# Performance work log

Measured on AMD Instinct MI355X. Metric: run time of the kernel, lower is better.

Reference implementation:

```python
import jax, jax.numpy as jnp
import numpy as np

LN_EPS = 1e-5

def _layernorm(x, g, b):
    mu = jnp.mean(x, axis=-1, keepdims=True)
    var = jnp.var(x, axis=-1, keepdims=True)
    return (x - mu) * jax.lax.rsqrt(var + LN_EPS) * g + b

def _attention(q_in, ctx, wq, wk, wv, wo, bo, n_heads):
    b, n, _ = q_in.shape
    m = ctx.shape[1]
    d_attn = wq.shape[1]
    d_head = d_attn // n_heads
    Q = (q_in @ wq).reshape(b, n, n_heads, d_head)
    K = (ctx @ wk).reshape(b, m, n_heads, d_head)
    V = (ctx @ wv).reshape(b, m, n_heads, d_head)
    scale = 1.0 / np.sqrt(d_head).astype(np.float32)
    sim = jnp.einsum('bnhd,bmhd->bhnm', Q, K) * scale
    attn = jax.nn.softmax(sim, axis=-1)
    out = jnp.einsum('bhnm,bmhd->bnhd', attn, V).reshape(b, n, d_attn)
    return out @ wo + bo

def setup_inputs() -> dict:
    key = jax.random.key(0)
    ks = jax.random.split(key, 16)
    B, N, D = 8, 1024, 640
    M, CD = 77, 768
    H = 4 * D  # GEGLU hidden = 2560
    s = lambda d: 1.0 / np.sqrt(d)
    return {
        'x': jax.random.normal(ks[0], (B, N, D), jnp.float32),
        'context': jax.random.normal(ks[1], (B, M, CD), jnp.float32),
        'sa_wq': jax.random.normal(ks[2], (D, D), jnp.float32) * s(D),
        'sa_wk': jax.random.normal(ks[3], (D, D), jnp.float32) * s(D),
        'sa_wv': jax.random.normal(ks[4], (D, D), jnp.float32) * s(D),
        'sa_wo': jax.random.normal(ks[5], (D, D), jnp.float32) * s(D),
        'sa_bo': jnp.zeros((D,), jnp.float32),
        'ca_wq': jax.random.normal(ks[6], (D, D), jnp.float32) * s(D),
        'ca_wk': jax.random.normal(ks[7], (CD, D), jnp.float32) * s(CD),
        'ca_wv': jax.random.normal(ks[8], (CD, D), jnp.float32) * s(CD),
        'ca_wo': jax.random.normal(ks[9], (D, D), jnp.float32) * s(D),
        'ca_bo': jnp.zeros((D,), jnp.float32),
        'ff_w1': jax.random.normal(ks[10], (D, 2 * H), jnp.float32) * s(D),
        'ff_b1': jnp.zeros((2 * H,), jnp.float32),
        'ff_w2': jax.random.normal(ks[11], (H, D), jnp.float32) * s(H),
        'ff_b2': jnp.zeros((D,), jnp.float32),
        'ln1_g': jnp.ones((D,), jnp.float32), 'ln1_b': jnp.zeros((D,), jnp.float32),
        'ln2_g': jnp.ones((D,), jnp.float32), 'ln2_b': jnp.zeros((D,), jnp.float32),
        'ln3_g': jnp.ones((D,), jnp.float32), 'ln3_b': jnp.zeros((D,), jnp.float32),
    }

def reference(x, context, sa_wq, sa_wk, sa_wv, sa_wo, sa_bo,
              ca_wq, ca_wk, ca_wv, ca_wo, ca_bo,
              ff_w1, ff_b1, ff_w2, ff_b2,
              ln1_g, ln1_b, ln2_g, ln2_b, ln3_g, ln3_b):
    n_heads = 8
    # post-norm residual block, matching norm_i(x + sublayer(x))
    x = _layernorm(x + _attention(x, x, sa_wq, sa_wk, sa_wv, sa_wo, sa_bo, n_heads), ln1_g, ln1_b)
    x = _layernorm(x + _attention(x, context, ca_wq, ca_wk, ca_wv, ca_wo, ca_bo, n_heads), ln2_g, ln2_b)
    h = x @ ff_w1 + ff_b1
    a, gate = jnp.split(h, 2, axis=-1)
    ff = (a * jax.nn.gelu(gate, approximate=False)) @ ff_w2 + ff_b2
    x = _layernorm(x + ff, ln3_g, ln3_b)
    return x
```

## Files before the change

kernel.cpp:

```cpp
#include <hip/hip_runtime.h>


using u16 = unsigned short;
typedef __attribute__((ext_vector_type(8))) short bfrag;
typedef __attribute__((ext_vector_type(4))) float f4;
typedef __attribute__((ext_vector_type(4))) unsigned short us4;

#define MFMA(a, b, c) __builtin_amdgcn_mfma_f32_16x16x32_bf16((a), (b), (c), 0, 0, 0)

__device__ __forceinline__ void gload16(const void* g, void* l) {
    __builtin_amdgcn_global_load_lds(
        (const __attribute__((address_space(1))) void*)g,
        (__attribute__((address_space(3))) void*)l, 16, 0, 0);
}

__device__ __forceinline__ u16 f2b(float f) {
    unsigned u = __float_as_uint(f);
    unsigned r = u + 0x7FFFu + ((u >> 16) & 1u);
    return (u16)(r >> 16);
}
__device__ __forceinline__ float b2f(u16 u) {
    return __uint_as_float(((unsigned)u) << 16);
}
__device__ __forceinline__ unsigned pack2(float a, float b) {
    return (unsigned)f2b(a) | ((unsigned)f2b(b) << 16);
}
__device__ __forceinline__ bfrag bzero() {
    bfrag z = {0,0,0,0,0,0,0,0};
    return z;
}
__device__ __forceinline__ float gelu_f(float x) {
    float y = 0.7978845608028654f * (x + 0.044715f * x * x * x);
    float e = exp2f(y * 2.8853900817779268f);
    float t = 1.0f - 2.0f * __builtin_amdgcn_rcpf(e + 1.0f);
    return 0.5f * x * (1.0f + t);
}

__device__ __forceinline__ void transp_tile(const float* __restrict__ in,
                                            u16* __restrict__ out,
                                            int K, int N, int ldo,
                                            int tile, bool perm,
                                            float (*t)[33])
{
    int nw = N >> 5;
    int n0 = (tile % nw) * 32, k0 = (tile / nw) * 32;
    int tx = threadIdx.x & 31, ty = threadIdx.x >> 5;
    #pragma unroll
    for (int i = 0; i < 32; i += 8)
        t[ty + i][tx] = in[(size_t)(k0 + ty + i) * N + n0 + tx];
    __syncthreads();
    #pragma unroll
    for (int i = 0; i < 32; i += 8) {
        int n = n0 + ty + i;
        int dst;
        if (perm) {
            dst = (n < 2560) ? ((n >> 5) * 64 + (n & 31))
                             : (((n - 2560) >> 5) * 64 + 32 + ((n - 2560) & 31));
        } else {
            dst = n;
        }
        out[(size_t)dst * ldo + k0 + tx] = f2b(t[tx][ty + i]);
    }
}

__global__ __launch_bounds__(256) void prep_k(
    const float* __restrict__ x, const float* __restrict__ ctx,
    const float* __restrict__ sa_wq, const float* __restrict__ sa_wk,
    const float* __restrict__ sa_wv, const float* __restrict__ sa_wo,
    const float* __restrict__ ca_wq, const float* __restrict__ ca_wk,
    const float* __restrict__ ca_wv, const float* __restrict__ ca_wo,
    const float* __restrict__ ff_w1, const float* __restrict__ ff_w2,
    u16* saqkvt, u16* sawot, u16* cawqt, u16* cawot, u16* cakvt,
    u16* ffw1t, u16* ffw2t, u16* xb, u16* ctxb)
{
    __shared__ float t[32][33];
    int b = blockIdx.x;
    if (b < 2400) {
        int task = b / 400, tile = b - task * 400;
        const float* src;
        u16* dst;
        if      (task == 0) { src = sa_wq; dst = saqkvt; }
        else if (task == 1) { src = sa_wk; dst = saqkvt + 409600; }
        else if (task == 2) { src = sa_wv; dst = saqkvt + 819200; }
        else if (task == 3) { src = sa_wo; dst = sawot; }
        else if (task == 4) { src = ca_wq; dst = cawqt; }
        else                { src = ca_wo; dst = cawot; }
        transp_tile(src, dst, 640, 640, 640, tile, false, t);
    } else if (b < 3360) {
        int tt = b - 2400;
        int task = tt / 480, tile = tt - task * 480;
        transp_tile(task ? ca_wv : ca_wk, cakvt + task * 491520, 768, 640, 768,
                    tile, false, t);
    } else if (b < 6560) {
        transp_tile(ff_w1, ffw1t, 640, 5120, 640, b - 3360, true, t);
    } else if (b < 8160) {
        transp_tile(ff_w2, ffw2t, 2560, 640, 2560, b - 6560, false, t);
    } else if (b < 10720) {
        int i = (b - 8160) * 256 + threadIdx.x;
        const float4* p = (const float4*)x + (size_t)i * 2;
        float4 a = p[0], bb = p[1];
        uint4 w = { pack2(a.x, a.y), pack2(a.z, a.w),
                    pack2(bb.x, bb.y), pack2(bb.z, bb.w) };
        ((uint4*)xb)[i] = w;
    } else {
        int i = (b - 10720) * 256 + threadIdx.x;
        int rowOut = i / 96, c8 = (i - rowOut * 96) * 8;
        int bb = rowOut / 80, r = rowOut - bb * 80;
        uint4 w = {0, 0, 0, 0};
        if (r < 77) {
            const float4* p = (const float4*)(ctx + ((size_t)(bb * 77 + r)) * 768 + c8);
            float4 a = p[0], b2 = p[1];
            w = (uint4){ pack2(a.x, a.y), pack2(a.z, a.w),
                         pack2(b2.x, b2.y), pack2(b2.z, b2.w) };
        }
        ((uint4*)ctxb)[i] = w;
    }
}

template<int MODE>
__device__ __forceinline__ void gemm_core(const u16* __restrict__ A,
                                          const u16* __restrict__ Bt,
                                          int N, int K, int ld,
                                          const float* __restrict__ bias,
                                          const u16* __restrict__ resb,
                                          float* __restrict__ outf,
                                          u16* __restrict__ outb,
                                          u16* __restrict__ out2,
                                          int bx, int by,
                                          u16* As, u16* Bs)
{
    const int lane = threadIdx.x & 63;
    const int wid  = threadIdx.x >> 6;
    const int q    = lane >> 4;
    const int lc   = lane & 15;
    const int wm = wid >> 1, wn = wid & 1;
    const int m0 = by * 128;
    const int n0 = bx * 128;
    const int ldb = ld * 2;

    f4 acc[4][4];
    #pragma unroll
    for (int i = 0; i < 4; ++i)
        #pragma unroll
        for (int j = 0; j < 4; ++j) acc[i][j] = (f4){0.f, 0.f, 0.f, 0.f};

    const char* Abase = (const char*)A + (size_t)m0 * ldb;
    const char* Bbase = (const char*)Bt + (size_t)n0 * ldb;

    for (int kt = 0; kt < K; kt += 64) {
        #pragma unroll
        for (int c = 0; c < 4; ++c) {
            int cid = wid * 4 + c;
            int o = cid * 1024 + lane * 16;
            int row = o >> 7;
            int pc  = o & 127;
            int src = pc ^ ((row & 7) << 4);
            gload16(Abase + (size_t)row * ldb + kt * 2 + src, (char*)As + cid * 1024);
            gload16(Bbase + (size_t)row * ldb + kt * 2 + src, (char*)Bs + cid * 1024);
        }
        __syncthreads();
        #pragma unroll
        for (int ks = 0; ks < 2; ++ks) {
            bfrag a[4], b[4];
            #pragma unroll
            for (int mi = 0; mi < 4; ++mi) {
                int row = wm * 64 + mi * 16 + lc;
                int off = row * 128 + ((ks * 64 + q * 16) ^ ((row & 7) << 4));
                a[mi] = *(const bfrag*)((const char*)As + off);
            }
            #pragma unroll
            for (int ni = 0; ni < 4; ++ni) {
                int row = wn * 64 + ni * 16 + lc;
                int off = row * 128 + ((ks * 64 + q * 16) ^ ((row & 7) << 4));
                b[ni] = *(const bfrag*)((const char*)Bs + off);
            }
            #pragma unroll
            for (int mi = 0; mi < 4; ++mi)
                #pragma unroll
                for (int ni = 0; ni < 4; ++ni)
                    acc[mi][ni] = MFMA(a[mi], b[ni], acc[mi][ni]);
        }
        __syncthreads();
    }

    const int baseRow = m0 + wm * 64;
    const int baseCol = n0 + wn * 64;

    if (MODE == 4) {
        const int blk = baseCol >> 6;
        #pragma unroll
        for (int mi = 0; mi < 4; ++mi)
            #pragma unroll
            for (int ni = 0; ni < 2; ++ni) {
                int j = blk * 32 + ni * 16 + lc;
                float ba = bias[j];
                float bg = bias[2560 + j];
                #pragma unroll
                for (int r = 0; r < 4; ++r) {
                    int row = baseRow + mi * 16 + q * 4 + r;
                    float aa = acc[mi][ni][r] + ba;
                    float gg = acc[mi][ni + 2][r] + bg;
                    outb[(size_t)row * 2560 + j] = f2b(aa * gelu_f(gg));
                }
            }
        return;
    }

    #pragma unroll
    for (int mi = 0; mi < 4; ++mi)
        #pragma unroll
        for (int ni = 0; ni < 4; ++ni) {
            int col = baseCol + ni * 16 + lc;
            if (MODE == 2) {
                const float qs = (col < 640) ? 0.11180339887498949f : 1.0f;
                us4 vv = {0, 0, 0, 0};
                #pragma unroll
                for (int r = 0; r < 4; ++r) {
                    int row = baseRow + mi * 16 + q * 4 + r;
                    u16 u = f2b(acc[mi][ni][r] * qs);
                    outb[(size_t)row * 1920 + col] = u;
                    vv[r] = u;
                }
                if (col >= 1280) {
                    int cd = col - 1280;
                    int hh = cd / 80, dd = cd - hh * 80;
                    int row0 = baseRow + mi * 16 + q * 4;
                    int bb = row0 >> 10, tok = row0 & 1023;
                    *(us4*)&out2[(size_t)((bb * 8 + hh) * 80 + dd) * 1024 + tok] = vv;
                }
            } else {
                #pragma unroll
                for (int r = 0; r < 4; ++r) {
                    int row = baseRow + mi * 16 + q * 4 + r;
                    float v = acc[mi][ni][r];
                    if (MODE == 1) {
                        outb[(size_t)row * N + col] = f2b(v);
                    } else if (MODE == 3) {
                        int bb = row / 80, rr = row - bb * 80;
                        if (rr < 77) {
                            u16 u = f2b(v);
                            if (col < 640) {
                                outb[(size_t)row * 640 + col] = u;
                            } else {
                                int cd = col - 640;
                                int hh = cd / 80, dd = cd - hh * 80;
                                out2[((bb * 8 + hh) * 80 + dd) * 80 + rr] = u;
                            }
                        }
                    }
                }
            }
        }
}

template<int MODE>
__global__ __launch_bounds__(256) void gemm_bt(const u16* __restrict__ A,
                                               const u16* __restrict__ Bt,
                                               int N, int K,
                                               const float* __restrict__ bias,
                                               const u16* __restrict__ resb,
                                               float* __restrict__ outf,
                                               u16* __restrict__ outb,
                                               u16* __restrict__ out2)
{
    __shared__ u16 As[128 * 64];
    __shared__ u16 Bs[128 * 64];
    gemm_core<MODE>(A, Bt, N, K, K, bias, resb, outf, outb, out2,
                    blockIdx.x, blockIdx.y, As, Bs);
}

__global__ __launch_bounds__(256) void gemm_qkv_cakv(
    const u16* __restrict__ xb, const u16* __restrict__ saqkvt,
    const u16* __restrict__ ctxb, const u16* __restrict__ cakvt,
    u16* qkvb, u16* vt, u16* kc, u16* vct)
{
    __shared__ u16 As[128 * 64];
    __shared__ u16 Bs[128 * 64];
    int bid = blockIdx.x;
    if (bid < 960) {
        gemm_core<2>(xb, saqkvt, 1920, 640, 640, nullptr, nullptr, nullptr,
                     qkvb, vt, bid % 15, bid / 15, As, Bs);
    } else {
        int tt = bid - 960;
        gemm_core<3>(ctxb, cakvt, 1280, 768, 768, nullptr, nullptr, nullptr,
                     kc, vct, tt % 10, tt / 10, As, Bs);
    }
}

template<int MODE>
__global__ __launch_bounds__(256) void gemm_n64(const u16* __restrict__ A,
                                                const u16* __restrict__ Bt,
                                                int N, int K,
                                                const float* __restrict__ bias,
                                                const u16* __restrict__ resb,
                                                u16* __restrict__ outb)
{
    __shared__ u16 As[128 * 64];
    __shared__ u16 Bs[64 * 64];
    const int lane = threadIdx.x & 63;
    const int wid  = threadIdx.x >> 6;
    const int hi   = lane >> 4;
    const int lc   = lane & 15;
    const int wm = wid >> 1, wn = wid & 1;
    const int m0 = blockIdx.y * 128;
    const int n0 = blockIdx.x * 64;
    const int ldb = K * 2;

    f4 acc[4][2];
    #pragma unroll
    for (int i = 0; i < 4; ++i)
        #pragma unroll
        for (int j = 0; j < 2; ++j) acc[i][j] = (f4){0.f, 0.f, 0.f, 0.f};

    const char* Abase = (const char*)A + (size_t)m0 * ldb;
    const char* Bbase = (const char*)Bt + (size_t)n0 * ldb;

    for (int kt = 0; kt < K; kt += 64) {
        #pragma unroll
        for (int c = 0; c < 6; ++c) {
            int cid = wid * 6 + c;
            if (cid < 16) {
                int o = cid * 1024 + lane * 16;
                int row = o >> 7;
                int src = (o & 127) ^ ((row & 7) << 4);
                gload16(Abase + (size_t)row * ldb + kt * 2 + src, (char*)As + cid * 1024);
            } else {
                int c2 = cid - 16;
                int o = c2 * 1024 + lane * 16;
                int row = o >> 7;
                int src = (o & 127) ^ ((row & 7) << 4);
                gload16(Bbase + (size_t)row * ldb + kt * 2 + src, (char*)Bs + c2 * 1024);
            }
        }
        __syncthreads();
        #pragma unroll
        for (int ks = 0; ks < 2; ++ks) {
            bfrag a[4], b[2];
            #pragma unroll
            for (int mi = 0; mi < 4; ++mi) {
                int row = wm * 64 + mi * 16 + lc;
                int off = row * 128 + ((ks * 64 + hi * 16) ^ ((row & 7) << 4));
                a[mi] = *(const bfrag*)((const char*)As + off);
            }
            #pragma unroll
            for (int ni = 0; ni < 2; ++ni) {
                int row = wn * 32 + ni * 16 + lc;
                int off = row * 128 + ((ks * 64 + hi * 16) ^ ((row & 7) << 4));
                b[ni] = *(const bfrag*)((const char*)Bs + off);
            }
            #pragma unroll
            for (int mi = 0; mi < 4; ++mi)
                #pragma unroll
                for (int ni = 0; ni < 2; ++ni)
                    acc[mi][ni] = MFMA(a[mi], b[ni], acc[mi][ni]);
        }
        __syncthreads();
    }

    const int baseRow = m0 + wm * 64;
    const int baseCol = n0 + wn * 32;
    #pragma unroll
    for (int mi = 0; mi < 4; ++mi)
        #pragma unroll
        for (int ni = 0; ni < 2; ++ni) {
            int col = baseCol + ni * 16 + lc;
            #pragma unroll
            for (int r = 0; r < 4; ++r) {
                int row = baseRow + mi * 16 + hi * 4 + r;
                float v = acc[mi][ni][r];
                if (MODE == 0)
                    v += bias[col] + b2f(resb[(size_t)row * N + col]);
                outb[(size_t)row * N + col] = f2b(v);
            }
        }
}

__global__ __launch_bounds__(256) void attn_sa(const u16* __restrict__ qkv,
                                               const u16* __restrict__ vt,
                                               u16* __restrict__ out)
{
    __shared__ u16 Qs[64 * 80];
    __shared__ u16 Ks[64 * 80];
    __shared__ u16 Vs[80 * 64];
    __shared__ u16 Ps[4][16 * 64];

    const int lane = threadIdx.x & 63;
    const int wid  = threadIdx.x >> 6;
    const int hi   = lane >> 4;
    const int lc   = lane & 15;
    const int bid = blockIdx.x;
    const int qt = bid >> 6;
    const int bb = (bid >> 3) & 7;
    const int hh = bid & 7;
    const int tok0 = bb * 1024 + qt * 64;
    const char* qbase = (const char*)qkv;

    for (int c = wid; c < 10; c += 4) {
        int o = c * 1024 + lane * 16;
        int row = o / 160, col = o - row * 160;
        gload16(qbase + (size_t)(tok0 + row) * 3840 + hh * 160 + col, (char*)Qs + c * 1024);
    }
    __syncthreads();

    const int qrow = wid * 16 + lc;
    bfrag qf0 = *(const bfrag*)((const char*)Qs + qrow * 160 + hi * 16);
    bfrag qf1 = *(const bfrag*)((const char*)Qs + qrow * 160 + 64 + hi * 16);
    bfrag qf2 = bzero();
    if (hi < 2) qf2 = *(const bfrag*)((const char*)Qs + qrow * 160 + 128 + hi * 16);

    float m = -3e30f, l = 0.f;
    f4 accO[5];
    #pragma unroll
    for (int no = 0; no < 5; ++no) accO[no] = (f4){0.f, 0.f, 0.f, 0.f};

    const float L2E = 1.4426950408889634f;

    for (int t = 0; t < 16; ++t) {
        __syncthreads();
        for (int c = wid; c < 20; c += 4) {
            if (c < 10) {
                int o = c * 1024 + lane * 16;
                int row = o / 160, col = o - row * 160;
                gload16(qbase + (size_t)(bb * 1024 + t * 64 + row) * 3840 + 1280 + hh * 160 + col,
                        (char*)Ks + c * 1024);
            } else {
                int c2 = c - 10;
                int o = c2 * 1024 + lane * 16;
                int row = o >> 7;
                int pc  = o & 127;
                int src = pc ^ ((row & 7) << 4);
                gload16((const char*)vt + (size_t)((bb * 8 + hh) * 80 + row) * 2048 + t * 128 + src,
                        (char*)Vs + c2 * 1024);
            }
        }
        __syncthreads();

        f4 sT[4];
        #pragma unroll
        for (int nb = 0; nb < 4; ++nb) {
            const char* kb = (const char*)Ks + (nb * 16 + lc) * 160;
            bfrag k0 = *(const bfrag*)(kb + hi * 16);
            bfrag k1 = *(const bfrag*)(kb + 64 + hi * 16);
            bfrag k2 = bzero();
            if (hi < 2) k2 = *(const bfrag*)(kb + 128 + hi * 16);
            f4 a = {0.f, 0.f, 0.f, 0.f};
            a = MFMA(k0, qf0, a);
            a = MFMA(k1, qf1, a);
            a = MFMA(k2, qf2, a);
            sT[nb] = a;
        }

        float pm = sT[0][0];
        #pragma unroll
        for (int nb = 0; nb < 4; ++nb)
            #pragma unroll
            for (int r = 0; r < 4; ++r) pm = fmaxf(pm, sT[nb][r]);
        pm = fmaxf(pm, __shfl_xor(pm, 16));
        pm = fmaxf(pm, __shfl_xor(pm, 32));

        if (__any(pm > m + 8.0f)) {
            float mn = fmaxf(m, pm);
            float al = exp2f((m - mn) * L2E);
            m = mn;
            l *= al;
            float af[4];
            #pragma unroll
            for (int r = 0; r < 4; ++r) af[r] = __shfl(al, hi * 4 + r);
            #pragma unroll
            for (int no = 0; no < 5; ++no)
                #pragma unroll
                for (int r = 0; r < 4; ++r) accO[no][r] *= af[r];
        }

        float sum = 0.f;
        #pragma unroll
        for (int nb = 0; nb < 4; ++nb)
            #pragma unroll
            for (int r = 0; r < 4; ++r) {
                float p = exp2f((sT[nb][r] - m) * L2E);
                sT[nb][r] = p;
                sum += p;
            }
        sum += __shfl_xor(sum, 16);
        sum += __shfl_xor(sum, 32);
        l += sum;

        char* Pw = (char*)&Ps[wid][0];
        #pragma unroll
        for (int nb = 0; nb < 4; ++nb) {
            us4 pk = { f2b(sT[nb][0]), f2b(sT[nb][1]), f2b(sT[nb][2]), f2b(sT[nb][3]) };
            int cb = (nb * 16 + hi * 4) * 2;
            *(us4*)(Pw + lc * 128 + (cb ^ ((lc & 7) << 4))) = pk;
        }

        bfrag pa0 = *(const bfrag*)(Pw + lc * 128 + ((hi * 16) ^ ((lc & 7) << 4)));
        bfrag pa1 = *(const bfrag*)(Pw + lc * 128 + ((64 + hi * 16) ^ ((lc & 7) << 4)));
        #pragma unroll
        for (int no = 0; no < 5; ++no) {
            int vr = no * 16 + lc;
            const char* vb = (const char*)Vs + vr * 128;
            bfrag v0 = *(const bfrag*)(vb + ((hi * 16) ^ ((vr & 7) << 4)));
            bfrag v1 = *(const bfrag*)(vb + ((64 + hi * 16) ^ ((vr & 7) << 4)));
            accO[no] = MFMA(pa0, v0, accO[no]);
            accO[no] = MFMA(pa1, v1, accO[no]);
        }
    }

    float rf[4];
    #pragma unroll
    for (int r = 0; r < 4; ++r) {
        float lf = __shfl(l, hi * 4 + r);
        rf[r] = __builtin_amdgcn_rcpf(lf);
    }
    #pragma unroll
    for (int no = 0; no < 5; ++no)
        #pragma unroll
        for (int r = 0; r < 4; ++r) {
            int row = tok0 + wid * 16 + hi * 4 + r;
            int col = hh * 80 + no * 16 + lc;
            out[(size_t)row * 640 + col] = f2b(accO[no][r] * rf[r]);
        }
}

__global__ __launch_bounds__(256) void attn_ca(const u16* __restrict__ qc,
                                               const u16* __restrict__ kc,
                                               const u16* __restrict__ vct,
                                               u16* __restrict__ out)
{
    __shared__ u16 Qs[64 * 80];
    __shared__ u16 Ks[84 * 80];
    __shared__ u16 Vs[84 * 80];
    __shared__ u16 Ps[4][16 * 80];

    const int lane = threadIdx.x & 63;
    const int wid  = threadIdx.x >> 6;
    const int q    = lane >> 4;
    const int lc   = lane & 15;
    const int bid = blockIdx.x;
    const int qt = bid & 15;
    const int hh = (bid >> 4) & 7;
    const int bb = bid >> 7;
    const int tok0 = bb * 1024 + qt * 64;

    for (int c = wid; c < 36; c += 4) {
        if (c < 10) {
            int o = c * 1024 + lane * 16;
            int row = o / 160, col = o - row * 160;
            gload16((const char*)qc + (size_t)(tok0 + row) * 1280 + hh * 160 + col,
                    (char*)Qs + c * 1024);
        } else if (c < 23) {
            int c2 = c - 10;
            int o = c2 * 1024 + lane * 16;
            int row = o / 160, col = o - row * 160;
            gload16((const char*)kc + (size_t)(bb * 80 + row) * 1280 + hh * 160 + col,
                    (char*)Ks + c2 * 1024);
        } else {
            int c2 = c - 23;
            int o = c2 * 1024 + lane * 16;
            int row = o / 160, col = o - row * 160;
            gload16((const char*)vct + (size_t)((bb * 8 + hh) * 80 + row) * 160 + col,
                    (char*)Vs + c2 * 1024);
        }
    }
    __syncthreads();

    const int qrow = wid * 16 + lc;
    bfrag qf0 = *(const bfrag*)((const char*)Qs + qrow * 160 + q * 16);
    bfrag qf1 = *(const bfrag*)((const char*)Qs + qrow * 160 + 64 + q * 16);
    bfrag qf2 = bzero();
    if (q < 2) qf2 = *(const bfrag*)((const char*)Qs + qrow * 160 + 128 + q * 16);

    const float SC = 0.11180339887498949f;
    const float L2E = 1.4426950408889634f;

    f4 s[5];
    #pragma unroll
    for (int nb = 0; nb < 5; ++nb) {
        const char* kb = (const char*)Ks + (nb * 16 + lc) * 160;
        bfrag k0 = *(const bfrag*)(kb + q * 16);
        bfrag k1 = *(const bfrag*)(kb + 64 + q * 16);
        bfrag k2 = bzero();
        if (q < 2) k2 = *(const bfrag*)(kb + 128 + q * 16);
        f4 a = {0.f, 0.f, 0.f, 0.f};
        a = MFMA(qf0, k0, a);
        a = MFMA(qf1, k1, a);
        a = MFMA(qf2, k2, a);
        s[nb] = a;
    }
    #pragma unroll
    for (int nb = 0; nb < 5; ++nb) {
        int key = nb * 16 + lc;
        #pragma unroll
        for (int r = 0; r < 4; ++r) {
            s[nb][r] *= SC;
            if (key >= 77) s[nb][r] = -1e30f;
        }
    }
    float mrow[4], lrow[4];
    #pragma unroll
    for (int r = 0; r < 4; ++r) {
        float v = fmaxf(fmaxf(fmaxf(s[0][r], s[1][r]), fmaxf(s[2][r], s[3][r])), s[4][r]);
        v = fmaxf(v, __shfl_xor(v, 1));
        v = fmaxf(v, __shfl_xor(v, 2));
        v = fmaxf(v, __shfl_xor(v, 4));
        v = fmaxf(v, __shfl_xor(v, 8));
        mrow[r] = v;
    }
    float rsum[4] = {0.f, 0.f, 0.f, 0.f};
    #pragma unroll
    for (int nb = 0; nb < 5; ++nb)
        #pragma unroll
        for (int r = 0; r < 4; ++r) {
            float p = exp2f((s[nb][r] - mrow[r]) * L2E);
            s[nb][r] = p;
            rsum[r] += p;
        }
    #pragma unroll
    for (int r = 0; r < 4; ++r) {
        float v = rsum[r];
        v += __shfl_xor(v, 1);
        v += __shfl_xor(v, 2);
        v += __shfl_xor(v, 4);
        v += __shfl_xor(v, 8);
        lrow[r] = v;
    }

    char* Pw = (char*)&Ps[wid][0];
    #pragma unroll
    for (int nb = 0; nb < 5; ++nb)
        #pragma unroll
        for (int r = 0; r < 4; ++r) {
            int prow = q * 4 + r;
            *(u16*)(Pw + prow * 160 + (nb * 16 + lc) * 2) = f2b(s[nb][r]);
        }
    bfrag pa0 = *(const bfrag*)(Pw + lc * 160 + q * 16);
    bfrag pa1 = *(const bfrag*)(Pw + lc * 160 + 64 + q * 16);
    bfrag pa2 = bzero();
    if (q < 2) pa2 = *(const bfrag*)(Pw + lc * 160 + 128 + q * 16);

    f4 accO[5];
    #pragma unroll
    for (int no = 0; no < 5; ++no) {
        const char* vb = (const char*)Vs + (no * 16 + lc) * 160;
        bfrag v0 = *(const bfrag*)(vb + q * 16);
        bfrag v1 = *(const bfrag*)(vb + 64 + q * 16);
        bfrag v2 = bzero();
        if (q < 2) v2 = *(const bfrag*)(vb + 128 + q * 16);
        f4 a = {0.f, 0.f, 0.f, 0.f};
        a = MFMA(pa0, v0, a);
        a = MFMA(pa1, v1, a);
        a = MFMA(pa2, v2, a);
        accO[no] = a;
    }
    #pragma unroll
    for (int no = 0; no < 5; ++no)
        #pragma unroll
        for (int r = 0; r < 4; ++r) {
            int row = tok0 + wid * 16 + q * 4 + r;
            int col = hh * 80 + no * 16 + lc;
            out[(size_t)row * 640 + col] = f2b(accO[no][r] / lrow[r]);
        }
}

__global__ __launch_bounds__(256) void ln_kb(const u16* __restrict__ pre,
                                             const float* __restrict__ g,
                                             const float* __restrict__ b,
                                             float* __restrict__ xo,
                                             u16* __restrict__ xb)
{
    const int lane = threadIdx.x & 63;
    const int wid  = threadIdx.x >> 6;
    const int row = blockIdx.x * 4 + wid;
    const u16* p = pre + (size_t)row * 640;
    float v[10];
    #pragma unroll
    for (int i = 0; i < 5; ++i) {
        unsigned d = *(const unsigned*)(p + i * 128 + lane * 2);
        v[2 * i]     = b2f((u16)(d & 0xffffu));
        v[2 * i + 1] = b2f((u16)(d >> 16));
    }
    float s = 0.f;
    #pragma unroll
    for (int i = 0; i < 10; ++i) s += v[i];
    #pragma unroll
    for (int m = 1; m < 64; m <<= 1) s += __shfl_xor(s, m);
    float mu = s * (1.0f / 640.0f);
    float d2 = 0.f;
    #pragma unroll
    for (int i = 0; i < 10; ++i) { float d = v[i] - mu; d2 += d * d; }
    #pragma unroll
    for (int m = 1; m < 64; m <<= 1) d2 += __shfl_xor(d2, m);
    float rs = rsqrtf(d2 * (1.0f / 640.0f) + 1e-5f);
    #pragma unroll
    for (int i = 0; i < 5; ++i) {
        int col = i * 128 + lane * 2;
        float y0 = (v[2 * i]     - mu) * rs * g[col]     + b[col];
        float y1 = (v[2 * i + 1] - mu) * rs * g[col + 1] + b[col + 1];
        if (xo) {
            *(float2*)&xo[(size_t)row * 640 + col] = make_float2(y0, y1);
        }
        if (xb) {
            *(unsigned*)&xb[(size_t)row * 640 + col] = pack2(y0, y1);
        }
    }
}

extern "C" void kernel_launch(void* const* d_in, const int* in_sizes, int n_in,
                              void* d_out, int out_size, void* d_ws, size_t ws_size,
                              hipStream_t stream)
{
    const float* x       = (const float*)d_in[0];
    const float* context = (const float*)d_in[1];
    const float* sa_wq = (const float*)d_in[2];
    const float* sa_wk = (const float*)d_in[3];
    const float* sa_wv = (const float*)d_in[4];
    const float* sa_wo = (const float*)d_in[5];
    const float* sa_bo = (const float*)d_in[6];
    const float* ca_wq = (const float*)d_in[7];
    const float* ca_wk = (const float*)d_in[8];
    const float* ca_wv = (const float*)d_in[9];
    const float* ca_wo = (const float*)d_in[10];
    const float* ca_bo = (const float*)d_in[11];
    const float* ff_w1 = (const float*)d_in[12];
    const float* ff_b1 = (const float*)d_in[13];
    const float* ff_w2 = (const float*)d_in[14];
    const float* ff_b2 = (const float*)d_in[15];
    const float* ln1_g = (const float*)d_in[16];
    const float* ln1_b = (const float*)d_in[17];
    const float* ln2_g = (const float*)d_in[18];
    const float* ln2_b = (const float*)d_in[19];
    const float* ln3_g = (const float*)d_in[20];
    const float* ln3_b = (const float*)d_in[21];

    char* ws = (char*)d_ws;
    const size_t OFF_XB     = 0;
    const size_t OFF_QKVB   = 10485760;
    const size_t OFF_VT     = 41943040;
    const size_t OFF_AB     = 52428800;
    const size_t OFF_ATTN   = 62914560;
    const size_t OFF_QC     = 73400320;
    const size_t OFF_KC     = 83886080;
    const size_t OFF_VCT    = 84705280;
    const size_t OFF_SAQKVT = 85524480;
    const size_t OFF_SAWOT  = 87982080;
    const size_t OFF_CAWQT  = 88801280;
    const size_t OFF_CAKVT  = 89620480;
    const size_t OFF_CAWOT  = 91586560;
    const size_t OFF_FFW1T  = 92405760;
    const size_t OFF_FFW2T  = 98959360;
    const size_t OFF_CTXB   = 102236160;
    const size_t OFF_PRE    = 103219200;

    u16* xb      = (u16*)(ws + OFF_XB);
    u16* qkvb    = (u16*)(ws + OFF_QKVB);
    u16* vt      = (u16*)(ws + OFF_VT);
    u16* ab      = (u16*)(ws + OFF_AB);
    u16* attnb   = (u16*)(ws + OFF_ATTN);
    u16* qc      = (u16*)(ws + OFF_QC);
    u16* kc      = (u16*)(ws + OFF_KC);
    u16* vct     = (u16*)(ws + OFF_VCT);
    u16* saqkvt  = (u16*)(ws + OFF_SAQKVT);
    u16* sawot   = (u16*)(ws + OFF_SAWOT);
    u16* cawqt   = (u16*)(ws + OFF_CAWQT);
    u16* cakvt   = (u16*)(ws + OFF_CAKVT);
    u16* cawot   = (u16*)(ws + OFF_CAWOT);
    u16* ffw1t   = (u16*)(ws + OFF_FFW1T);
    u16* ffw2t   = (u16*)(ws + OFF_FFW2T);
    u16* ctxb    = (u16*)(ws + OFF_CTXB);
    u16* psum    = (u16*)(ws + OFF_PRE);
    u16* ffh     = (u16*)(ws + OFF_XB);

    hipLaunchKernelGGL(prep_k, dim3(10960), dim3(256), 0, stream,
                       x, context, sa_wq, sa_wk, sa_wv, sa_wo, ca_wq, ca_wk,
                       ca_wv, ca_wo, ff_w1, ff_w2,
                       saqkvt, sawot, cawqt, cawot, cakvt, ffw1t, ffw2t, xb, ctxb);

    hipLaunchKernelGGL(gemm_qkv_cakv, dim3(1010), dim3(256), 0, stream,
                       xb, saqkvt, ctxb, cakvt, qkvb, vt, kc, vct);
    hipLaunchKernelGGL(attn_sa, dim3(1024), dim3(256), 0, stream, qkvb, vt, attnb);
    hipLaunchKernelGGL(gemm_n64<0>, dim3(10, 64), dim3(256), 0, stream,
                       attnb, sawot, 640, 640, sa_bo, xb, psum);
    hipLaunchKernelGGL(ln_kb, dim3(2048), dim3(256), 0, stream, psum, ln1_g, ln1_b,
                       (float*)nullptr, ab);

    hipLaunchKernelGGL(gemm_n64<1>, dim3(10, 64), dim3(256), 0, stream,
                       ab, cawqt, 640, 640, (const float*)nullptr, (const u16*)nullptr,
                       qc);
    hipLaunchKernelGGL(attn_ca, dim3(1024), dim3(256), 0, stream, qc, kc, vct, attnb);
    hipLaunchKernelGGL(gemm_n64<0>, dim3(10, 64), dim3(256), 0, stream,
                       attnb, cawot, 640, 640, ca_bo, ab, psum);
    hipLaunchKernelGGL(ln_kb, dim3(2048), dim3(256), 0, stream, psum, ln2_g, ln2_b,
                       (float*)nullptr, ab);

    hipLaunchKernelGGL(gemm_bt<4>, dim3(40, 64), dim3(256), 0, stream,
                       ab, ffw1t, 5120, 640, ff_b1, (const u16*)nullptr,
                       (float*)nullptr, ffh, (u16*)nullptr);
    hipLaunchKernelGGL(gemm_n64<0>, dim3(10, 64), dim3(256), 0, stream,
                       ffh, ffw2t, 640, 2560, ff_b2, ab, psum);
    hipLaunchKernelGGL(ln_kb, dim3(2048), dim3(256), 0, stream, psum, ln3_g, ln3_b,
                       (float*)d_out, (u16*)nullptr);
}
```

Baseline: 342.4 us.

## Prefetch next K/V tile into registers during self-attention compute

Replaces the per-iteration direct global-to-LDS loads of the K and V tiles with register prefetching. The next tile is loaded into registers at the start of each iteration and written to LDS after compute finishes. Loop-invariant address setup is precomputed once per thread. The aim is to hide global load latency behind the MFMA work, at the cost of extra VGPRs and a register-staging path that no longer uses the direct LDS load instruction.

```diff
diff --git a/kernel.cpp b/kernel.cpp
--- a/kernel.cpp
+++ b/kernel.cpp
@@ -400,6 +400,50 @@
         int row = o / 160, col = o - row * 160;
         gload16(qbase + (size_t)(tok0 + row) * 3840 + hh * 160 + col, (char*)Qs + c * 1024);
     }
+
+    const char* gsrc0; const char* gsrc1; const char* gsrc2;
+    const char* gsrc3; const char* gsrc4;
+    char* ldst0; char* ldst1; char* ldst2; char* ldst3; char* ldst4;
+    size_t tstep0, tstep1, tstep2, tstep3, tstep4;
+    {
+        const char* kbase = qbase + (size_t)(bb * 1024) * 3840 + 1280 + hh * 160;
+        const char* vbase = (const char*)vt + (size_t)((bb * 8 + hh) * 80) * 2048;
+#define SETUP_CH(I)                                                            \
+        {                                                                      \
+            int c = wid + 4 * I;                                               \
+            if (c < 10) {                                                      \
+                int o = c * 1024 + lane * 16;                                  \
+                int row = o / 160, col = o - row * 160;                        \
+                gsrc##I = kbase + (size_t)row * 3840 + col;                    \
+                tstep##I = (size_t)64 * 3840;                                  \
+                ldst##I = (char*)Ks + c * 1024 + lane * 16;                    \
+            } else {                                                           \
+                int c2 = c - 10;                                               \
+                int o = c2 * 1024 + lane * 16;                                 \
+                int row = o >> 7;                                              \
+                int src = (o & 127) ^ ((row & 7) << 4);                        \
+                gsrc##I = vbase + (size_t)row * 2048 + src;                    \
+                tstep##I = 128;                                                \
+                ldst##I = (char*)Vs + c2 * 1024 + lane * 16;                   \
+            }                                                                  \
+        }
+        SETUP_CH(0) SETUP_CH(1) SETUP_CH(2) SETUP_CH(3) SETUP_CH(4)
+#undef SETUP_CH
+    }
+
+    uint4 pf0, pf1, pf2, pf3, pf4;
+#define LD_TILE(T)                                                             \
+    pf0 = *(const uint4*)(gsrc0 + (size_t)(T) * tstep0);                       \
+    pf1 = *(const uint4*)(gsrc1 + (size_t)(T) * tstep1);                       \
+    pf2 = *(const uint4*)(gsrc2 + (size_t)(T) * tstep2);                       \
+    pf3 = *(const uint4*)(gsrc3 + (size_t)(T) * tstep3);                       \
+    pf4 = *(const uint4*)(gsrc4 + (size_t)(T) * tstep4);
+#define ST_TILE()                                                              \
+    *(uint4*)ldst0 = pf0; *(uint4*)ldst1 = pf1; *(uint4*)ldst2 = pf2;          \
+    *(uint4*)ldst3 = pf3; *(uint4*)ldst4 = pf4;
+
+    LD_TILE(0)
+    ST_TILE()
     __syncthreads();
 
     const int qrow = wid * 16 + lc;
@@ -416,24 +460,7 @@
     const float L2E = 1.4426950408889634f;
 
     for (int t = 0; t < 16; ++t) {
-        __syncthreads();
-        for (int c = wid; c < 20; c += 4) {
-            if (c < 10) {
-                int o = c * 1024 + lane * 16;
-                int row = o / 160, col = o - row * 160;
-                gload16(qbase + (size_t)(bb * 1024 + t * 64 + row) * 3840 + 1280 + hh * 160 + col,
-                        (char*)Ks + c * 1024);
-            } else {
-                int c2 = c - 10;
-                int o = c2 * 1024 + lane * 16;
-                int row = o >> 7;
-                int pc  = o & 127;
-                int src = pc ^ ((row & 7) << 4);
-                gload16((const char*)vt + (size_t)((bb * 8 + hh) * 80 + row) * 2048 + t * 128 + src,
-                        (char*)Vs + c2 * 1024);
-            }
-        }
-        __syncthreads();
+        if (t < 15) { LD_TILE(t + 1) }
 
         f4 sT[4];
         #pragma unroll
@@ -504,7 +531,15 @@
             accO[no] = MFMA(pa0, v0, accO[no]);
             accO[no] = MFMA(pa1, v1, accO[no]);
         }
-    }
+
+        __syncthreads();
+        if (t < 15) {
+            ST_TILE()
+            __syncthreads();
+        }
+    }
+#undef LD_TILE
+#undef ST_TILE
 
     float rf[4];
     #pragma unroll
```

Result: no change. 338.2 us (-1.2%).
